# Performance work log

Hardware: AMD Instinct MI355X
Metric: run time of the kernel (lower is better)

The kernel has to match this reference:

```python
import jax, jax.numpy as jnp
import numpy as np

DIM = 768
HEADS = 12
DIM_HEAD = DIM // HEADS
FACTOR = DIM_HEAD ** (-0.5)
B, T = 4, 2048


def setup_inputs() -> dict:
    key = jax.random.key(0)
    k1, k2, k3 = jax.random.split(key, 3)
    x = jax.random.normal(k1, (B, T, DIM), dtype=jnp.float32)
    # VarianceScaling-like init scale for linear weights
    W_qkv = jax.random.normal(k2, (DIM, 3 * DIM), dtype=jnp.float32) * (DIM ** -0.5)
    W_out = jax.random.normal(k3, (DIM, DIM), dtype=jnp.float32) * (DIM ** -0.5)
    return {"x": x, "W_qkv": W_qkv, "W_out": W_out}


def reference(x, W_qkv, W_out):
    b, t, _ = x.shape
    qkv = x @ W_qkv  # [b, t, 3*dim]
    # einops 'b t (d k h) -> k b h t d' with k=3, h=HEADS: d slowest, k middle, h fastest
    qkv = qkv.reshape(b, t, DIM_HEAD, 3, HEADS)
    qkv = jnp.transpose(qkv, (3, 0, 4, 1, 2))  # [3, b, h, t, d]
    q, k, v = qkv[0], qkv[1], qkv[2]
    # scaled dot-product attention, full [b,h,t,t] scores as in the original
    scores = jnp.einsum('bhid,bhjd->bhij', q, k) * FACTOR
    attn = jax.nn.softmax(scores, axis=-1)
    out = jnp.einsum('bhij,bhjd->bhid', attn, v)  # [b, h, t, d]
    # 'b h t d -> b t (h d)'
    out = jnp.transpose(out, (0, 2, 1, 3)).reshape(b, t, HEADS * DIM_HEAD)
    return out @ W_out
```

## Files before the change

### kernel.cpp

```cpp
#include <hip/hip_runtime.h>
#include <hip/hip_bf16.h>

#define DIM    768
#define HEADS  12
#define DHEAD  64
#define BATCH  4
#define SEQ    2048
#define NROW   (BATCH * SEQ)
#define QKVN   (3 * DIM)
#define FACTOR 0.125f
#define QSCALE 0.18033688011112042f

typedef __attribute__((ext_vector_type(8))) short short8;
typedef __attribute__((ext_vector_type(4))) float floatx4;

__device__ __forceinline__ floatx4 mfma16(short8 a, short8 b, floatx4 c) {
    return __builtin_amdgcn_mfma_f32_16x16x32_bf16(a, b, c, 0, 0, 0);
}

__device__ __forceinline__ void glds16(const void* g, void* l) {
    __builtin_amdgcn_global_load_lds((const __attribute__((address_space(1))) void*)g,
                                     (__attribute__((address_space(3))) void*)l,
                                     16, 0, 0);
}

__device__ __forceinline__ short rne16(float f) {
    unsigned u = __builtin_bit_cast(unsigned, f);
    return (short)((u + 0x7fffu + ((u >> 16) & 1u)) >> 16);
}
__device__ __forceinline__ unsigned pack2(float lo, float hi) {
    unsigned ul = __builtin_bit_cast(unsigned, lo);
    unsigned uh = __builtin_bit_cast(unsigned, hi);
    ul = (ul + 0x7fffu + ((ul >> 16) & 1u)) >> 16;
    uh = (uh + 0x7fffu + ((uh >> 16) & 1u)) & 0xffff0000u;
    return ul | uh;
}

__device__ __forceinline__ int swz8(int row, int col) {
    return (row << 6) + ((((col >> 3) ^ row) & 7) << 3) + (col & 7);
}

__global__ __launch_bounds__(256) void conv_bf16(const float* __restrict__ x,
                                                 short* __restrict__ xb) {
    int g = blockIdx.x * 256 + threadIdx.x;
    float4 v = ((const float4*)x)[g];
    uint2 o;
    o.x = pack2(v.x, v.y);
    o.y = pack2(v.z, v.w);
    ((uint2*)xb)[g] = o;
}

__global__ __launch_bounds__(256) void transpose_w(const float* __restrict__ W,
                                                   short* __restrict__ Wt,
                                                   int K, int N, int permute) {
    __shared__ short T[32][33];
    int n0 = blockIdx.x * 32, k0 = blockIdx.y * 32;
    int c = threadIdx.x & 31, r0 = threadIdx.x >> 5;
    for (int r = r0; r < 32; r += 8)
        T[r][c] = rne16(W[(size_t)(k0 + r) * N + n0 + c]);
    __syncthreads();
    for (int r = r0; r < 32; r += 8) {
        int n = n0 + r;
        int np;
        if (permute) {
            int d = n / 36, rem = n - d * 36;
            int which = rem / 12, h = rem - which * 12;
            np = which * 768 + h * 64 + d;
        } else {
            np = n;
        }
        Wt[(size_t)np * K + k0 + c] = T[c][r];
    }
}

__global__ __launch_bounds__(256) void gemm_qkv(const short* __restrict__ A,
                                                const short* __restrict__ Bt,
                                                short* __restrict__ Qo,
                                                short* __restrict__ Ko,
                                                short* __restrict__ Vto) {
    __shared__ short As[128 * 64];
    __shared__ short Bs[128 * 64];
    const int tid = threadIdx.x;
    const int lane = tid & 63, wave = tid >> 6;
    const int l15 = lane & 15, quad = lane >> 4;

    const int flat = blockIdx.x;
    const int xcd = flat & 7;
    const int local = flat >> 3;
    const int mloc = local & 7, nloc = local >> 3;
    const int m0 = (xcd * 8 + mloc) * 128;
    const int n0 = nloc * 128;

    const int wm = (wave >> 1) * 64, wn = (wave & 1) * 64;
    const int r8 = wave * 8 + (lane >> 3);
    const int c8 = lane & 7;
    const int sc = ((c8 ^ (r8 & 7)) << 3);

    floatx4 acc[4][4] = {};
    for (int k0 = 0; k0 < DIM; k0 += 64) {
#pragma unroll
        for (int i = 0; i < 4; ++i) {
            int row = i * 32 + r8;
            glds16(&A[(size_t)(m0 + row) * DIM + k0 + sc], &As[(size_t)(i * 32 + wave * 8) * 64]);
            glds16(&Bt[(size_t)(n0 + row) * DIM + k0 + sc], &Bs[(size_t)(i * 32 + wave * 8) * 64]);
        }
        __syncthreads();
#pragma unroll
        for (int ks = 0; ks < 2; ++ks) {
            short8 a[4], b[4];
#pragma unroll
            for (int mt = 0; mt < 4; ++mt)
                a[mt] = *(const short8*)&As[swz8(wm + mt * 16 + l15, ks * 32 + quad * 8)];
#pragma unroll
            for (int nt = 0; nt < 4; ++nt)
                b[nt] = *(const short8*)&Bs[swz8(wn + nt * 16 + l15, ks * 32 + quad * 8)];
#pragma unroll
            for (int mt = 0; mt < 4; ++mt)
#pragma unroll
                for (int nt = 0; nt < 4; ++nt)
                    acc[mt][nt] = mfma16(a[mt], b[nt], acc[mt][nt]);
        }
        __syncthreads();
    }

    const int sn = n0 + wn;
    const int which = sn / 768;
    const int h = (sn - which * 768) >> 6;
    const int bb = (m0 + wm) >> 11;
    const int tbase = (m0 + wm) & 2047;
    const size_t tilebase = ((size_t)(bb * HEADS + h) * 32 + (tbase >> 6)) * 4096;

    if (which != 2) {
        short* dst = (which == 0) ? Qo : Ko;
        const float scale = (which == 0) ? QSCALE : 1.0f;
#pragma unroll
        for (int mt = 0; mt < 4; ++mt)
#pragma unroll
            for (int nt = 0; nt < 4; ++nt) {
                int d = nt * 16 + l15;
#pragma unroll
                for (int r = 0; r < 4; ++r) {
                    int tl = mt * 16 + quad * 4 + r;
                    dst[tilebase + swz8(tl, d)] = rne16(acc[mt][nt][r] * scale);
                }
            }
    } else {
        short* vld = ((wave < 2) ? As : Bs) + (wave & 1) * 4096;
#pragma unroll
        for (int mt = 0; mt < 4; ++mt)
#pragma unroll
            for (int nt = 0; nt < 4; ++nt) {
                int d = nt * 16 + l15;
                int tl = mt * 16 + quad * 4;
                int chunk = (tl >> 3) ^ (d & 7);
                int addr = (d << 6) + (chunk << 3) + (tl & 7);
                uint2 pk;
                pk.x = pack2(acc[mt][nt][0], acc[mt][nt][1]);
                pk.y = pack2(acc[mt][nt][2], acc[mt][nt][3]);
                *(uint2*)&vld[addr] = pk;
            }
    }
    __syncthreads();
    if (which == 2) {
        short* vld = ((wave < 2) ? As : Bs) + (wave & 1) * 4096;
#pragma unroll
        for (int i = 0; i < 8; ++i) {
            int c = (i * 64 + lane) * 8;
            *(uint4*)&Vto[tilebase + c] = *(const uint4*)&vld[c];
        }
    }
}

__global__ __launch_bounds__(512, 6) void attn_mfma(const short* __restrict__ Q,
                                                    const short* __restrict__ K,
                                                    const short* __restrict__ Vt,
                                                    short* __restrict__ O) {
    __shared__ __align__(16) short buf[8192];
    __shared__ __align__(16) short Ps[8192];

    const int tid = threadIdx.x;
    const int lane = tid & 63, wave = tid >> 6;
    const int l15 = lane & 15, quad = lane >> 4;
    const int flat = blockIdx.x;
    const int xcd = flat & 7, li = flat >> 3;
    const int bh = xcd + (li % 6) * 8;
    const int q0 = (li / 6) * 128;
    const size_t base = (size_t)bh * SEQ * DHEAD;
    const int wr = wave * 16;
    short* myP = Ps + wave * 1024;
    short* Ks = buf;
    short* Vs = buf + 4096;
    const int lane8 = lane * 8;

    {
        size_t qtb = base + (size_t)(q0 >> 6) * 4096;
#pragma unroll
        for (int i = 0; i < 2; ++i)
            glds16(&Q[qtb + (size_t)(i * 8 + wave) * 512 + lane8],
                   &buf[(i * 8 + wave) * 512]);
    }
    __syncthreads();
    short8 qf[2];
#pragma unroll
    for (int ks = 0; ks < 2; ++ks)
        qf[ks] = *(const short8*)&buf[swz8(wr + l15, ks * 32 + quad * 8)];
    __syncthreads();

    floatx4 o[4] = {};
    float lsum = 0.f;

    for (int j0 = 0; j0 < SEQ; j0 += 64) {
        size_t ktb = base + (size_t)(j0 >> 6) * 4096 + wave * 512 + lane8;
        glds16(&K[ktb], &Ks[wave * 512]);
        glds16(&Vt[ktb], &Vs[wave * 512]);
        __syncthreads();

        floatx4 s[4] = {};
#pragma unroll
        for (int ks = 0; ks < 2; ++ks) {
            short8 kf[4];
#pragma unroll
            for (int kt = 0; kt < 4; ++kt)
                kf[kt] = *(const short8*)&Ks[swz8(kt * 16 + l15, ks * 32 + quad * 8)];
#pragma unroll
            for (int kt = 0; kt < 4; ++kt)
                s[kt] = mfma16(kf[kt], qf[ks], s[kt]);
        }

#pragma unroll
        for (int kt = 0; kt < 4; ++kt) {
            float p0 = __builtin_amdgcn_exp2f(s[kt][0]);
            float p1 = __builtin_amdgcn_exp2f(s[kt][1]);
            float p2 = __builtin_amdgcn_exp2f(s[kt][2]);
            float p3 = __builtin_amdgcn_exp2f(s[kt][3]);
            lsum += (p0 + p1) + (p2 + p3);
            uint2 pk;
            pk.x = pack2(p0, p1);
            pk.y = pack2(p2, p3);
            *(uint2*)&myP[swz8(l15, kt * 16 + quad * 4)] = pk;
        }

#pragma unroll
        for (int ks = 0; ks < 2; ++ks) {
            short8 a = *(const short8*)&myP[swz8(l15, ks * 32 + quad * 8)];
            short8 b[4];
#pragma unroll
            for (int dt = 0; dt < 4; ++dt)
                b[dt] = *(const short8*)&Vs[swz8(dt * 16 + l15, ks * 32 + quad * 8)];
#pragma unroll
            for (int dt = 0; dt < 4; ++dt)
                o[dt] = mfma16(a, b[dt], o[dt]);
        }
        __syncthreads();
    }

    const int b = bh / HEADS, h = bh - b * HEADS;
    float rs = lsum;
    rs += __shfl_xor(rs, 16);
    rs += __shfl_xor(rs, 32);
    float invl = 1.f / rs;
#pragma unroll
    for (int r = 0; r < 4; ++r) {
        float inv = __shfl(invl, quad * 4 + r);
        int t = q0 + wr + quad * 4 + r;
#pragma unroll
        for (int dt = 0; dt < 4; ++dt) {
            int d = dt * 16 + l15;
            O[((size_t)(b * SEQ + t)) * DIM + h * DHEAD + d] = rne16(o[dt][r] * inv);
        }
    }
}

__global__ __launch_bounds__(256) void gemm_out(const short* __restrict__ A,
                                                const short* __restrict__ Bt,
                                                float* __restrict__ out) {
    __shared__ short As[128 * 64];
    __shared__ short Bs[128 * 64];
    const int tid = threadIdx.x;
    const int lane = tid & 63, wave = tid >> 6;
    const int l15 = lane & 15, quad = lane >> 4;
    const int m0 = blockIdx.y * 128, n0 = blockIdx.x * 128;
    const int wm = (wave >> 1) * 64, wn = (wave & 1) * 64;
    const int r8 = wave * 8 + (lane >> 3);
    const int sc = (((lane & 7) ^ (r8 & 7)) << 3);

    floatx4 acc[4][4] = {};
    for (int k0 = 0; k0 < DIM; k0 += 64) {
#pragma unroll
        for (int i = 0; i < 4; ++i) {
            int row = i * 32 + r8;
            glds16(&A[(size_t)(m0 + row) * DIM + k0 + sc], &As[(size_t)(i * 32 + wave * 8) * 64]);
            glds16(&Bt[(size_t)(n0 + row) * DIM + k0 + sc], &Bs[(size_t)(i * 32 + wave * 8) * 64]);
        }
        __syncthreads();
#pragma unroll
        for (int ks = 0; ks < 2; ++ks) {
            short8 a[4], b[4];
#pragma unroll
            for (int mt = 0; mt < 4; ++mt)
                a[mt] = *(const short8*)&As[swz8(wm + mt * 16 + l15, ks * 32 + quad * 8)];
#pragma unroll
            for (int nt = 0; nt < 4; ++nt)
                b[nt] = *(const short8*)&Bs[swz8(wn + nt * 16 + l15, ks * 32 + quad * 8)];
#pragma unroll
            for (int mt = 0; mt < 4; ++mt)
#pragma unroll
                for (int nt = 0; nt < 4; ++nt)
                    acc[mt][nt] = mfma16(a[mt], b[nt], acc[mt][nt]);
        }
        __syncthreads();
    }

#pragma unroll
    for (int mt = 0; mt < 4; ++mt)
#pragma unroll
        for (int nt = 0; nt < 4; ++nt)
#pragma unroll
            for (int r = 0; r < 4; ++r) {
                int m = m0 + wm + mt * 16 + quad * 4 + r;
                int n = n0 + wn + nt * 16 + l15;
                out[(size_t)m * DIM + n] = acc[mt][nt][r];
            }
}

extern "C" void kernel_launch(void* const* d_in, const int* in_sizes, int n_in,
                              void* d_out, int out_size, void* d_ws, size_t ws_size,
                              hipStream_t stream) {
    const float* x    = (const float*)d_in[0];
    const float* Wqkv = (const float*)d_in[1];
    const float* Wout = (const float*)d_in[2];
    float* out = (float*)d_out;

    const size_t NE = (size_t)NROW * DIM;
    short* xb  = (short*)d_ws;
    short* Wqt = xb + NE;
    short* Wot = Wqt + (size_t)QKVN * DIM;
    short* Qw  = Wot + (size_t)DIM * DIM;
    short* Kw  = Qw + NE;
    short* Vtw = Kw + NE;

    conv_bf16<<<NE / 4 / 256, 256, 0, stream>>>(x, xb);
    transpose_w<<<dim3(QKVN / 32, DIM / 32), 256, 0, stream>>>(Wqkv, Wqt, DIM, QKVN, 1);
    transpose_w<<<dim3(DIM / 32, DIM / 32), 256, 0, stream>>>(Wout, Wot, DIM, DIM, 0);
    gemm_qkv<<<8 * 8 * 18, 256, 0, stream>>>(xb, Wqt, Qw, Kw, Vtw);
    attn_mfma<<<768, 512, 0, stream>>>(Qw, Kw, Vtw, xb);
    gemm_out<<<dim3(DIM / 128, NROW / 128), 256, 0, stream>>>(xb, Wot, out);
}
```

Before: 225.6 us.

## Split attention tiles across wave pairs, sharing P through LDS

Each pair of waves now owns 32 query rows instead of each wave owning 16. Within a pair, each wave computes scores for half of the key block and the output for half of the head dimension. The probability tile is exchanged through shared memory, and row sums are combined through a small LDS buffer at the end. This cuts per-wave LDS fragment reads for K and V through register reuse, but adds an extra block-wide barrier in every key iteration.

After: 225.9 us. Within noise of the previous version (+0.1%).

```diff
diff --git a/kernel.cpp b/kernel.cpp
--- a/kernel.cpp
+++ b/kernel.cpp
@@ -177,19 +177,20 @@
                                                     short* __restrict__ O) {
     __shared__ __align__(16) short buf[8192];
     __shared__ __align__(16) short Ps[8192];
+    __shared__ float Lx[256];
 
     const int tid = threadIdx.x;
     const int lane = tid & 63, wave = tid >> 6;
     const int l15 = lane & 15, quad = lane >> 4;
+    const int pair = wave >> 1, sh = wave & 1;
     const int flat = blockIdx.x;
     const int xcd = flat & 7, li = flat >> 3;
     const int bh = xcd + (li % 6) * 8;
     const int q0 = (li / 6) * 128;
     const size_t base = (size_t)bh * SEQ * DHEAD;
-    const int wr = wave * 16;
-    short* myP = Ps + wave * 1024;
     short* Ks = buf;
     short* Vs = buf + 4096;
+    short* Pp = Ps + pair * 2048;
     const int lane8 = lane * 8;
 
     {
@@ -200,14 +201,17 @@
                    &buf[(i * 8 + wave) * 512]);
     }
     __syncthreads();
-    short8 qf[2];
-#pragma unroll
-    for (int ks = 0; ks < 2; ++ks)
-        qf[ks] = *(const short8*)&buf[swz8(wr + l15, ks * 32 + quad * 8)];
-    __syncthreads();
-
-    floatx4 o[4] = {};
-    float lsum = 0.f;
+    short8 qf[2][2];
+#pragma unroll
+    for (int mt = 0; mt < 2; ++mt)
+#pragma unroll
+        for (int ks = 0; ks < 2; ++ks)
+            qf[mt][ks] = *(const short8*)&buf[swz8(pair * 32 + mt * 16 + l15,
+                                                   ks * 32 + quad * 8)];
+    __syncthreads();
+
+    floatx4 o[2][2] = {};
+    float lsum[2] = {0.f, 0.f};
 
     for (int j0 = 0; j0 < SEQ; j0 += 64) {
         size_t ktb = base + (size_t)(j0 >> 6) * 4096 + wave * 512 + lane8;
@@ -215,58 +219,70 @@
         glds16(&Vt[ktb], &Vs[wave * 512]);
         __syncthreads();
 
-        floatx4 s[4] = {};
+        floatx4 sa[2][2] = {};
 #pragma unroll
         for (int ks = 0; ks < 2; ++ks) {
-            short8 kf[4];
-#pragma unroll
-            for (int kt = 0; kt < 4; ++kt)
-                kf[kt] = *(const short8*)&Ks[swz8(kt * 16 + l15, ks * 32 + quad * 8)];
-#pragma unroll
-            for (int kt = 0; kt < 4; ++kt)
-                s[kt] = mfma16(kf[kt], qf[ks], s[kt]);
-        }
-
-#pragma unroll
-        for (int kt = 0; kt < 4; ++kt) {
-            float p0 = __builtin_amdgcn_exp2f(s[kt][0]);
-            float p1 = __builtin_amdgcn_exp2f(s[kt][1]);
-            float p2 = __builtin_amdgcn_exp2f(s[kt][2]);
-            float p3 = __builtin_amdgcn_exp2f(s[kt][3]);
-            lsum += (p0 + p1) + (p2 + p3);
-            uint2 pk;
-            pk.x = pack2(p0, p1);
-            pk.y = pack2(p2, p3);
-            *(uint2*)&myP[swz8(l15, kt * 16 + quad * 4)] = pk;
-        }
+            short8 kf0 = *(const short8*)&Ks[swz8(sh * 32 + l15, ks * 32 + quad * 8)];
+            short8 kf1 = *(const short8*)&Ks[swz8(sh * 32 + 16 + l15, ks * 32 + quad * 8)];
+            sa[0][0] = mfma16(kf0, qf[0][ks], sa[0][0]);
+            sa[0][1] = mfma16(kf1, qf[0][ks], sa[0][1]);
+            sa[1][0] = mfma16(kf0, qf[1][ks], sa[1][0]);
+            sa[1][1] = mfma16(kf1, qf[1][ks], sa[1][1]);
+        }
+
+#pragma unroll
+        for (int mt = 0; mt < 2; ++mt)
+#pragma unroll
+            for (int kt = 0; kt < 2; ++kt) {
+                float p0 = __builtin_amdgcn_exp2f(sa[mt][kt][0]);
+                float p1 = __builtin_amdgcn_exp2f(sa[mt][kt][1]);
+                float p2 = __builtin_amdgcn_exp2f(sa[mt][kt][2]);
+                float p3 = __builtin_amdgcn_exp2f(sa[mt][kt][3]);
+                lsum[mt] += (p0 + p1) + (p2 + p3);
+                uint2 pk;
+                pk.x = pack2(p0, p1);
+                pk.y = pack2(p2, p3);
+                *(uint2*)&Pp[swz8(mt * 16 + l15, sh * 32 + kt * 16 + quad * 4)] = pk;
+            }
+        __syncthreads();
 
 #pragma unroll
         for (int ks = 0; ks < 2; ++ks) {
-            short8 a = *(const short8*)&myP[swz8(l15, ks * 32 + quad * 8)];
-            short8 b[4];
-#pragma unroll
-            for (int dt = 0; dt < 4; ++dt)
-                b[dt] = *(const short8*)&Vs[swz8(dt * 16 + l15, ks * 32 + quad * 8)];
-#pragma unroll
-            for (int dt = 0; dt < 4; ++dt)
-                o[dt] = mfma16(a, b[dt], o[dt]);
-        }
-        __syncthreads();
-    }
+            short8 a0 = *(const short8*)&Pp[swz8(l15, ks * 32 + quad * 8)];
+            short8 a1 = *(const short8*)&Pp[swz8(16 + l15, ks * 32 + quad * 8)];
+            short8 b0 = *(const short8*)&Vs[swz8(sh * 32 + l15, ks * 32 + quad * 8)];
+            short8 b1 = *(const short8*)&Vs[swz8(sh * 32 + 16 + l15, ks * 32 + quad * 8)];
+            o[0][0] = mfma16(a0, b0, o[0][0]);
+            o[0][1] = mfma16(a0, b1, o[0][1]);
+            o[1][0] = mfma16(a1, b0, o[1][0]);
+            o[1][1] = mfma16(a1, b1, o[1][1]);
+        }
+        __syncthreads();
+    }
+
+    float r0 = lsum[0], r1 = lsum[1];
+    r0 += __shfl_xor(r0, 16); r0 += __shfl_xor(r0, 32);
+    r1 += __shfl_xor(r1, 16); r1 += __shfl_xor(r1, 32);
+    if (quad == 0) {
+        Lx[pair * 64 + sh * 32 + l15] = r0;
+        Lx[pair * 64 + sh * 32 + 16 + l15] = r1;
+    }
+    __syncthreads();
+    float inv0 = 1.f / (r0 + Lx[pair * 64 + (sh ^ 1) * 32 + l15]);
+    float inv1 = 1.f / (r1 + Lx[pair * 64 + (sh ^ 1) * 32 + 16 + l15]);
 
     const int b = bh / HEADS, h = bh - b * HEADS;
-    float rs = lsum;
-    rs += __shfl_xor(rs, 16);
-    rs += __shfl_xor(rs, 32);
-    float invl = 1.f / rs;
 #pragma unroll
     for (int r = 0; r < 4; ++r) {
-        float inv = __shfl(invl, quad * 4 + r);
-        int t = q0 + wr + quad * 4 + r;
-#pragma unroll
-        for (int dt = 0; dt < 4; ++dt) {
-            int d = dt * 16 + l15;
-            O[((size_t)(b * SEQ + t)) * DIM + h * DHEAD + d] = rne16(o[dt][r] * inv);
+        float iv0 = __shfl(inv0, quad * 4 + r);
+        float iv1 = __shfl(inv1, quad * 4 + r);
+#pragma unroll
+        for (int mt = 0; mt < 2; ++mt) {
+            int t = q0 + pair * 32 + mt * 16 + quad * 4 + r;
+            float iv = mt ? iv1 : iv0;
+            size_t rowo = ((size_t)(b * SEQ + t)) * DIM + h * DHEAD + sh * 32;
+            O[rowo + l15] = rne16(o[mt][0][r] * iv);
+            O[rowo + 16 + l15] = rne16(o[mt][1][r] * iv);
         }
     }
 }
```
